# Kernel tuning notes

Hardware: AMD Instinct MI355X
Metric: run time of the kernel (lower is better)

Reference implementation:

```python
import jax, jax.numpy as jnp
import numpy as np

S, N, L, D, H, V = 64, 128, 10, 300, 150, 50000


def setup_inputs() -> dict:
    key = jax.random.key(0)
    k0, k1, k2, k3 = jax.random.split(key, 4)
    tokens = jax.random.randint(k0, (S, N), 0, V)
    emb_table = jax.random.normal(k1, (V, D), jnp.float32) * 0.02
    W1 = jax.random.normal(k2, (D, H), jnp.float32) * (1.0 / np.sqrt(D))
    b1 = jnp.zeros((H,), jnp.float32)
    W2 = jax.random.normal(k3, (H, 1), jnp.float32) * (1.0 / np.sqrt(H))
    b2 = jnp.zeros((1,), jnp.float32)
    return {"tokens": tokens, "emb_table": emb_table, "W1": W1, "b1": b1, "W2": W2, "b2": b2}


def reference(tokens, emb_table, W1, b1, W2, b2):
    # word embeddings per sentence: [S, N, D]
    emb = emb_table[tokens]
    # FFNN attention score per token: Linear->ReLU->Linear(->1), squeeze -> [S, N]
    scores = (jax.nn.relu(emb @ W1 + b1) @ W2 + b2)[..., 0]

    n = tokens.shape[1]
    k = jnp.arange(L)                      # window position within span
    pos = jnp.arange(n)
    idx = pos[:, None] + k[None, :]        # [N, L] absolute token index of span (i, i+k)
    valid = idx < n                        # span position in-bounds
    idx_c = jnp.minimum(idx, n - 1)

    win_emb = emb[:, idx_c]                # [S, N, L, D]  emb[s, i+k]
    win_sc = scores[:, idx_c]              # [S, N, L]     scores[s, i+k]

    # tri[w, k] = (k <= w): positions belonging to span of width index w
    tri = k[:, None] >= k[None, :]                       # [L, L]
    m = tri[None, None] & valid[None, :, None, :]        # [1, N, L(w), L(k)]
    logits = jnp.where(m, win_sc[:, :, None, :], -jnp.inf)
    probs = jax.nn.softmax(logits, axis=-1)              # [S, N, Lw, Lk]
    head = jnp.einsum('snwk,snkd->snwd', probs, win_emb)  # softmax-weighted sum

    first = jnp.broadcast_to(emb[:, :, None, :], win_emb.shape)  # emb[i]
    last = win_emb                                               # emb[i+w] at k-axis == w
    out = jnp.concatenate([first, last, head], axis=-1)          # [S, N, L, 3D]
    # zero out spans that run past the sentence end
    return out * valid[None, :, :, None].astype(out.dtype)
```

## Files before the change

### kernel.cpp

```cpp
#include <hip/hip_runtime.h>
#include <cstddef>

#define SS 64
#define NN 128
#define LL 10
#define DD 300
#define HH 150
#define HP 160
#define CC 16
#define RMAX (CC + LL - 1)

#define WS_SC  0
#define WS_W1P (WS_SC + SS*NN)
#define WS_BW  (WS_W1P + DD*HP)

typedef float vf4 __attribute__((ext_vector_type(4)));

__device__ __forceinline__ void fma4(float4& a, float s, const float4 b) {
    a.x = fmaf(s, b.x, a.x);
    a.y = fmaf(s, b.y, a.y);
    a.z = fmaf(s, b.z, a.z);
    a.w = fmaf(s, b.w, a.w);
}

__device__ __forceinline__ void nt_store4(float* p, const float4 v) {
    vf4 t = {v.x, v.y, v.z, v.w};
    __builtin_nontemporal_store(t, (vf4*)p);
}

__global__ void pad_weights(const float* __restrict__ W1, const float* __restrict__ b1,
                            const float* __restrict__ W2, float* __restrict__ W1p,
                            float* __restrict__ bW) {
    int idx = blockIdx.x * 256 + threadIdx.x;
    if (idx < DD * HP) {
        int d = idx / HP, j = idx - d * HP;
        W1p[idx] = (j < HH) ? W1[d * HH + j] : 0.f;
    }
    if (idx < HP) {
        bW[idx] = (idx < HH) ? b1[idx] : 0.f;
    } else if (idx < 2 * HP) {
        int j = idx - HP;
        bW[idx] = (j < HH) ? W2[j] : 0.f;
    }
}

constexpr int TB = 32;

__global__ __launch_bounds__(256) void k_scores(
        const int* __restrict__ tokens, const float* __restrict__ table,
        const float* __restrict__ W1p, const float* __restrict__ bW,
        const float* __restrict__ b2, float* __restrict__ ws_sc)
{
    __shared__ float lemb[TB][DD + 4];
    __shared__ float lpart[TB][40];
    __shared__ int   ltok[TB];

    const int tid = threadIdx.x;
    const int t0  = blockIdx.x * TB;

    if (tid < TB) ltok[tid] = tokens[t0 + tid];
    __syncthreads();

    for (int l = tid; l < TB * 75; l += 256) {
        const int t = l / 75, q = l - t * 75;
        *(float4*)&lemb[t][q * 4] = *(const float4*)(table + (size_t)ltok[t] * DD + q * 4);
    }
    __syncthreads();

    for (int slot = tid; slot < 8 * 38; slot += 256) {
        const int tg = slot / 38;
        const int jg = slot - tg * 38;
        const int j0 = jg * 4;
        const int tt = tg * 4;

        float4 acc0 = {0,0,0,0}, acc1 = {0,0,0,0}, acc2 = {0,0,0,0}, acc3 = {0,0,0,0};
        const float* wp = W1p + j0;

        #pragma unroll 5
        for (int d = 0; d < DD; d += 4) {
            const float4 e0 = *(const float4*)&lemb[tt + 0][d];
            const float4 e1 = *(const float4*)&lemb[tt + 1][d];
            const float4 e2 = *(const float4*)&lemb[tt + 2][d];
            const float4 e3 = *(const float4*)&lemb[tt + 3][d];
            const float4 w0 = *(const float4*)(wp + (size_t)(d + 0) * HP);
            const float4 w1 = *(const float4*)(wp + (size_t)(d + 1) * HP);
            const float4 w2 = *(const float4*)(wp + (size_t)(d + 2) * HP);
            const float4 w3 = *(const float4*)(wp + (size_t)(d + 3) * HP);
            fma4(acc0, e0.x, w0); fma4(acc0, e0.y, w1); fma4(acc0, e0.z, w2); fma4(acc0, e0.w, w3);
            fma4(acc1, e1.x, w0); fma4(acc1, e1.y, w1); fma4(acc1, e1.z, w2); fma4(acc1, e1.w, w3);
            fma4(acc2, e2.x, w0); fma4(acc2, e2.y, w1); fma4(acc2, e2.z, w2); fma4(acc2, e2.w, w3);
            fma4(acc3, e3.x, w0); fma4(acc3, e3.y, w1); fma4(acc3, e3.z, w2); fma4(acc3, e3.w, w3);
        }

        const float4 bb = *(const float4*)(bW + j0);
        const float4 v2 = *(const float4*)(bW + HP + j0);

        #define RELD(A) (fmaxf((A).x + bb.x, 0.f) * v2.x + \
                         fmaxf((A).y + bb.y, 0.f) * v2.y + \
                         fmaxf((A).z + bb.z, 0.f) * v2.z + \
                         fmaxf((A).w + bb.w, 0.f) * v2.w)
        lpart[tt + 0][jg] = RELD(acc0);
        lpart[tt + 1][jg] = RELD(acc1);
        lpart[tt + 2][jg] = RELD(acc2);
        lpart[tt + 3][jg] = RELD(acc3);
        #undef RELD
    }
    __syncthreads();

    if (tid < TB) {
        float s = 0.f;
        #pragma unroll
        for (int jg = 0; jg < 38; ++jg) s += lpart[tid][jg];
        ws_sc[t0 + tid] = s + b2[0];
    }
}

__global__ __launch_bounds__(256) void k_out(
        const int* __restrict__ tokens, const float* __restrict__ table,
        const float* __restrict__ ws_sc, float* __restrict__ out)
{
    const int bid = blockIdx.x;
    const int s   = bid >> 3;
    const int i0  = (bid & 7) * CC;
    const int R   = min(RMAX, NN - i0);

    __shared__ float le[RMAX][DD + 4];
    __shared__ float lp[CC][LL][12];
    __shared__ float sc_l[RMAX];

    const int tid = threadIdx.x;

    if (tid < R) sc_l[tid] = ws_sc[s * NN + i0 + tid];

    const int* tk = tokens + s * NN + i0;
    for (int l = tid; l < R * 75; l += 256) {
        const int k = l / 75, q = l - k * 75;
        *(float4*)&le[k][q * 4] = *(const float4*)(table + (size_t)tk[k] * DD + q * 4);
    }
    __syncthreads();

    if (tid < CC * LL) {
        const int li = tid / LL, w = tid - li * LL;
        const int nk = min(LL, NN - (i0 + li));
        if (w < nk) {
            float m = -1e30f;
            for (int k = 0; k <= w; ++k) m = fmaxf(m, sc_l[li + k]);
            float sum = 0.f;
            for (int k = 0; k <= w; ++k) sum += __expf(sc_l[li + k] - m);
            const float inv = 1.f / sum;
            for (int k = 0; k <= w; ++k) lp[li][w][k] = __expf(sc_l[li + k] - m) * inv;
        }
    }
    __syncthreads();

    float* dst = out + (size_t)(s * NN + i0) * (LL * 3 * DD);
    for (int o4 = tid; o4 < CC * 2250; o4 += 256) {
        const int li = o4 / 2250;
        const int r  = o4 - li * 2250;
        const int w  = r / 225;
        const int c4 = r - w * 225;
        const int c  = c4 * 4;
        const int nk = min(LL, NN - (i0 + li));
        float4 v;
        if (w >= nk) {
            v = make_float4(0.f, 0.f, 0.f, 0.f);
        } else if (c < DD) {
            v = *(const float4*)&le[li][c];
        } else if (c < 2 * DD) {
            v = *(const float4*)&le[li + w][c - DD];
        } else {
            const int cc = c - 2 * DD;
            float4 a = make_float4(0.f, 0.f, 0.f, 0.f);
            for (int k = 0; k <= w; ++k) {
                fma4(a, lp[li][w][k], *(const float4*)&le[li + k][cc]);
            }
            v = a;
        }
        nt_store4(dst + (size_t)o4 * 4, v);
    }
}

extern "C" void kernel_launch(void* const* d_in, const int* in_sizes, int n_in,
                              void* d_out, int out_size, void* d_ws, size_t ws_size,
                              hipStream_t stream) {
    const int*   tokens = (const int*)d_in[0];
    const float* table  = (const float*)d_in[1];
    const float* W1     = (const float*)d_in[2];
    const float* b1     = (const float*)d_in[3];
    const float* W2     = (const float*)d_in[4];
    const float* b2     = (const float*)d_in[5];
    float* out = (float*)d_out;
    float* ws  = (float*)d_ws;

    float* ws_sc = ws + WS_SC;
    float* W1p   = ws + WS_W1P;
    float* bW    = ws + WS_BW;

    pad_weights<<<(DD * HP + 255) / 256, 256, 0, stream>>>(W1, b1, W2, W1p, bW);
    k_scores<<<(SS * NN) / TB, 256, 0, stream>>>(tokens, table, W1p, bW, b2, ws_sc);
    k_out<<<SS * (NN / CC), 256, 0, stream>>>(tokens, table, ws_sc, out);
}
```

Before: 121.8 us.

## Fuse score MLP into output kernel, recomputing halo scores per block

The separate score kernel is removed. Each output block now computes the FFNN scores for its own 16 tokens plus the 9-token halo, reusing the embeddings it already loads into shared memory, then runs the softmax and output write. This drops one kernel launch and the score round trip through global memory, at the cost of recomputing halo scores (about 25 rows per block instead of 16). W1 padding shrinks from 160 to 152 columns, and the matvec is retiled to 2 tokens × 8 hidden units per thread, which leaves more work per thread on only 247 active threads.

```diff
diff --git a/kernel.cpp b/kernel.cpp
--- a/kernel.cpp
+++ b/kernel.cpp
@@ -6,13 +6,14 @@
 #define LL 10
 #define DD 300
 #define HH 150
-#define HP 160
+#define HP 152
 #define CC 16
 #define RMAX (CC + LL - 1)
+#define JG 19
+#define TG 13
 
-#define WS_SC  0
-#define WS_W1P (WS_SC + SS*NN)
-#define WS_BW  (WS_W1P + DD*HP)
+#define WS_W1P 0
+#define WS_BW  (DD*HP)
 
 typedef float vf4 __attribute__((ext_vector_type(4)));
 
@@ -44,80 +45,10 @@
     }
 }
 
-constexpr int TB = 32;
-
-__global__ __launch_bounds__(256) void k_scores(
+__global__ __launch_bounds__(256) void k_fused(
         const int* __restrict__ tokens, const float* __restrict__ table,
         const float* __restrict__ W1p, const float* __restrict__ bW,
-        const float* __restrict__ b2, float* __restrict__ ws_sc)
-{
-    __shared__ float lemb[TB][DD + 4];
-    __shared__ float lpart[TB][40];
-    __shared__ int   ltok[TB];
-
-    const int tid = threadIdx.x;
-    const int t0  = blockIdx.x * TB;
-
-    if (tid < TB) ltok[tid] = tokens[t0 + tid];
-    __syncthreads();
-
-    for (int l = tid; l < TB * 75; l += 256) {
-        const int t = l / 75, q = l - t * 75;
-        *(float4*)&lemb[t][q * 4] = *(const float4*)(table + (size_t)ltok[t] * DD + q * 4);
-    }
-    __syncthreads();
-
-    for (int slot = tid; slot < 8 * 38; slot += 256) {
-        const int tg = slot / 38;
-        const int jg = slot - tg * 38;
-        const int j0 = jg * 4;
-        const int tt = tg * 4;
-
-        float4 acc0 = {0,0,0,0}, acc1 = {0,0,0,0}, acc2 = {0,0,0,0}, acc3 = {0,0,0,0};
-        const float* wp = W1p + j0;
-
-        #pragma unroll 5
-        for (int d = 0; d < DD; d += 4) {
-            const float4 e0 = *(const float4*)&lemb[tt + 0][d];
-            const float4 e1 = *(const float4*)&lemb[tt + 1][d];
-            const float4 e2 = *(const float4*)&lemb[tt + 2][d];
-            const float4 e3 = *(const float4*)&lemb[tt + 3][d];
-            const float4 w0 = *(const float4*)(wp + (size_t)(d + 0) * HP);
-            const float4 w1 = *(const float4*)(wp + (size_t)(d + 1) * HP);
-            const float4 w2 = *(const float4*)(wp + (size_t)(d + 2) * HP);
-            const float4 w3 = *(const float4*)(wp + (size_t)(d + 3) * HP);
-            fma4(acc0, e0.x, w0); fma4(acc0, e0.y, w1); fma4(acc0, e0.z, w2); fma4(acc0, e0.w, w3);
-            fma4(acc1, e1.x, w0); fma4(acc1, e1.y, w1); fma4(acc1, e1.z, w2); fma4(acc1, e1.w, w3);
-            fma4(acc2, e2.x, w0); fma4(acc2, e2.y, w1); fma4(acc2, e2.z, w2); fma4(acc2, e2.w, w3);
-            fma4(acc3, e3.x, w0); fma4(acc3, e3.y, w1); fma4(acc3, e3.z, w2); fma4(acc3, e3.w, w3);
-        }
-
-        const float4 bb = *(const float4*)(bW + j0);
-        const float4 v2 = *(const float4*)(bW + HP + j0);
-
-        #define RELD(A) (fmaxf((A).x + bb.x, 0.f) * v2.x + \
-                         fmaxf((A).y + bb.y, 0.f) * v2.y + \
-                         fmaxf((A).z + bb.z, 0.f) * v2.z + \
-                         fmaxf((A).w + bb.w, 0.f) * v2.w)
-        lpart[tt + 0][jg] = RELD(acc0);
-        lpart[tt + 1][jg] = RELD(acc1);
-        lpart[tt + 2][jg] = RELD(acc2);
-        lpart[tt + 3][jg] = RELD(acc3);
-        #undef RELD
-    }
-    __syncthreads();
-
-    if (tid < TB) {
-        float s = 0.f;
-        #pragma unroll
-        for (int jg = 0; jg < 38; ++jg) s += lpart[tid][jg];
-        ws_sc[t0 + tid] = s + b2[0];
-    }
-}
-
-__global__ __launch_bounds__(256) void k_out(
-        const int* __restrict__ tokens, const float* __restrict__ table,
-        const float* __restrict__ ws_sc, float* __restrict__ out)
+        const float* __restrict__ b2, float* __restrict__ out)
 {
     const int bid = blockIdx.x;
     const int s   = bid >> 3;
@@ -126,16 +57,73 @@
 
     __shared__ float le[RMAX][DD + 4];
     __shared__ float lp[CC][LL][12];
+    __shared__ float lpart[RMAX][20];
     __shared__ float sc_l[RMAX];
+    __shared__ int   ltok[RMAX];
 
     const int tid = threadIdx.x;
 
-    if (tid < R) sc_l[tid] = ws_sc[s * NN + i0 + tid];
+    if (tid < R) ltok[tid] = tokens[s * NN + i0 + tid];
+    __syncthreads();
 
-    const int* tk = tokens + s * NN + i0;
     for (int l = tid; l < R * 75; l += 256) {
-        const int k = l / 75, q = l - k * 75;
-        *(float4*)&le[k][q * 4] = *(const float4*)(table + (size_t)tk[k] * DD + q * 4);
+        const int t = l / 75, q = l - t * 75;
+        *(float4*)&le[t][q * 4] = *(const float4*)(table + (size_t)ltok[t] * DD + q * 4);
+    }
+    __syncthreads();
+
+    if (tid < TG * JG) {
+        const int tg = tid / JG;
+        const int jg = tid - tg * JG;
+        const int t0 = tg * 2;
+        if (t0 < R) {
+            const int t1 = (t0 + 1 < R) ? (t0 + 1) : t0;
+            const int j0 = jg * 8;
+            const float* wp = W1p + j0;
+
+            float4 a0l = {0,0,0,0}, a0h = {0,0,0,0}, a1l = {0,0,0,0}, a1h = {0,0,0,0};
+            #pragma unroll 5
+            for (int d = 0; d < DD; d += 4) {
+                const float4 e0 = *(const float4*)&le[t0][d];
+                const float4 e1 = *(const float4*)&le[t1][d];
+                const float4 wa0 = *(const float4*)(wp + (size_t)(d + 0) * HP);
+                const float4 wb0 = *(const float4*)(wp + (size_t)(d + 0) * HP + 4);
+                const float4 wa1 = *(const float4*)(wp + (size_t)(d + 1) * HP);
+                const float4 wb1 = *(const float4*)(wp + (size_t)(d + 1) * HP + 4);
+                const float4 wa2 = *(const float4*)(wp + (size_t)(d + 2) * HP);
+                const float4 wb2 = *(const float4*)(wp + (size_t)(d + 2) * HP + 4);
+                const float4 wa3 = *(const float4*)(wp + (size_t)(d + 3) * HP);
+                const float4 wb3 = *(const float4*)(wp + (size_t)(d + 3) * HP + 4);
+                fma4(a0l, e0.x, wa0); fma4(a0h, e0.x, wb0);
+                fma4(a0l, e0.y, wa1); fma4(a0h, e0.y, wb1);
+                fma4(a0l, e0.z, wa2); fma4(a0h, e0.z, wb2);
+                fma4(a0l, e0.w, wa3); fma4(a0h, e0.w, wb3);
+                fma4(a1l, e1.x, wa0); fma4(a1h, e1.x, wb0);
+                fma4(a1l, e1.y, wa1); fma4(a1h, e1.y, wb1);
+                fma4(a1l, e1.z, wa2); fma4(a1h, e1.z, wb2);
+                fma4(a1l, e1.w, wa3); fma4(a1h, e1.w, wb3);
+            }
+            const float4 bl = *(const float4*)(bW + j0);
+            const float4 bh = *(const float4*)(bW + j0 + 4);
+            const float4 vl = *(const float4*)(bW + HP + j0);
+            const float4 vh = *(const float4*)(bW + HP + j0 + 4);
+
+            #define RELD(A, B, V) (fmaxf((A).x + (B).x, 0.f) * (V).x + \
+                                   fmaxf((A).y + (B).y, 0.f) * (V).y + \
+                                   fmaxf((A).z + (B).z, 0.f) * (V).z + \
+                                   fmaxf((A).w + (B).w, 0.f) * (V).w)
+            lpart[t0][jg] = RELD(a0l, bl, vl) + RELD(a0h, bh, vh);
+            if (t0 + 1 < R) lpart[t0 + 1][jg] = RELD(a1l, bl, vl) + RELD(a1h, bh, vh);
+            #undef RELD
+        }
+    }
+    __syncthreads();
+
+    if (tid < R) {
+        float sum = 0.f;
+        #pragma unroll
+        for (int jg = 0; jg < JG; ++jg) sum += lpart[tid][jg];
+        sc_l[tid] = sum + b2[0];
     }
     __syncthreads();
 
@@ -192,11 +180,9 @@
     float* out = (float*)d_out;
     float* ws  = (float*)d_ws;
 
-    float* ws_sc = ws + WS_SC;
-    float* W1p   = ws + WS_W1P;
-    float* bW    = ws + WS_BW;
+    float* W1p = ws + WS_W1P;
+    float* bW  = ws + WS_BW;
 
     pad_weights<<<(DD * HP + 255) / 256, 256, 0, stream>>>(W1, b1, W2, W1p, bW);
-    k_scores<<<(SS * NN) / TB, 256, 0, stream>>>(tokens, table, W1p, bW, b2, ws_sc);
-    k_out<<<SS * (NN / CC), 256, 0, stream>>>(tokens, table, ws_sc, out);
+    k_fused<<<SS * (NN / CC), 256, 0, stream>>>(tokens, table, W1p, bW, b2, out);
 }
```

New measurement: 116.5 us. -4.3%, faster.
